# Optimization experiments

Hardware: AMD Instinct MI355X
Metric: run time of the kernel (lower is better)

The kernel has to match this reference:

```python
import jax, jax.numpy as jnp
import numpy as np

N_NODES = 100000
N_EDGES = 1600000
N_GRAPHS = 512
NUM_REL = 3


def setup_inputs() -> dict:
    key = jax.random.key(0)
    ks = jax.random.split(key, 16)
    shape_idx = jax.random.randint(ks[0], (N_NODES,), 0, 16)
    color_idx = jax.random.randint(ks[1], (N_NODES,), 0, 8)
    node_feats = jnp.stack([shape_idx, color_idx], axis=1)  # [N,2] int
    edge_index = jax.random.randint(ks[2], (2, N_EDGES), 0, N_NODES)
    edge_type = jax.random.randint(ks[3], (N_EDGES,), 0, NUM_REL)
    batch = jnp.sort(jax.random.randint(ks[4], (N_NODES,), 0, N_GRAPHS))
    s = lambda k, sh: jax.random.normal(k, sh, dtype=jnp.float32) * 0.05
    return {
        'node_feats': node_feats,
        'edge_index': edge_index,
        'edge_type': edge_type,
        'batch': batch,
        'shape_emb': s(ks[5], (16, 8)),
        'color_emb': s(ks[6], (8, 8)),
        'pre_w': s(ks[7], (16, 32)),
        'pre_b': jnp.zeros((32,), jnp.float32),
        'root1': s(ks[8], (32, 64)),
        'rel1': s(ks[9], (NUM_REL, 32, 64)),
        'bias1': jnp.zeros((64,), jnp.float32),
        'root2': s(ks[10], (64, 64)),
        'rel2': s(ks[11], (NUM_REL, 64, 64)),
        'bias2': jnp.zeros((64,), jnp.float32),
        'cls_w': s(ks[12], (64, 10)),
        'cls_b': jnp.zeros((10,), jnp.float32),
    }


def rgcn_conv(x, edge_index, edge_type, root, rel_w, bias):
    # PyG RGCNConv: out_i = x_i @ root + sum_r mean_{j in N_r(i)} x_j @ W_r + bias
    src, dst = edge_index[0], edge_index[1]
    out = x @ root + bias
    xs = x[src]  # [E, in] gathered source features
    for r in range(NUM_REL):
        m = (edge_type == r).astype(x.dtype)  # [E]
        msg = (xs @ rel_w[r]) * m[:, None]  # [E, out]
        agg = jax.ops.segment_sum(msg, dst, num_segments=N_NODES)
        cnt = jax.ops.segment_sum(m, dst, num_segments=N_NODES)
        out = out + agg / jnp.maximum(cnt, 1.0)[:, None]
    return out


def reference(node_feats, edge_index, edge_type, batch, shape_emb, color_emb,
              pre_w, pre_b, root1, rel1, bias1, root2, rel2, bias2, cls_w, cls_b):
    x = jnp.concatenate([shape_emb[node_feats[:, 0]], color_emb[node_feats[:, 1]]], axis=1)  # [N,16]
    x = jax.nn.relu(x @ pre_w + pre_b)  # [N,32]
    x = jax.nn.relu(rgcn_conv(x, edge_index, edge_type, root1, rel1, bias1))  # [N,64]
    x = jax.nn.relu(rgcn_conv(x, edge_index, edge_type, root2, rel2, bias2))  # [N,64]
    # global_mean_pool over graph ids
    s = jax.ops.segment_sum(x, batch, num_segments=N_GRAPHS)
    c = jax.ops.segment_sum(jnp.ones((x.shape[0],), x.dtype), batch, num_segments=N_GRAPHS)
    pooled = s / jnp.maximum(c, 1.0)[:, None]  # [G,64]
    return pooled @ cls_w + cls_b  # [G,num_classes]
```

## Files before the change

kernel.cpp:

```cpp
#include <hip/hip_runtime.h>

#define NN 100000
#define NE 1600000
#define NG 512

#define BSH 9
#define NB 196
#define EPB 8192
#define NAB ((NE + EPB - 1) / EPB)
#define CAP 9216

__global__ __launch_bounds__(256) void k_embed(
    const int* __restrict__ nf, const float* __restrict__ semb,
    const float* __restrict__ cemb, const float* __restrict__ pw,
    const float* __restrict__ pb, float* __restrict__ x1)
{
  int gid = blockIdx.x * 256 + threadIdx.x;
  bool valid = gid < NN;
  int i = valid ? gid : NN - 1;
  int sf = nf[2 * i], cf = nf[2 * i + 1];
  float x0[16];
#pragma unroll
  for (int k = 0; k < 8; ++k) x0[k] = semb[sf * 8 + k];
#pragma unroll
  for (int k = 0; k < 8; ++k) x0[8 + k] = cemb[cf * 8 + k];
  float acc[32];
#pragma unroll
  for (int j = 0; j < 32; ++j) acc[j] = pb[j];
#pragma unroll
  for (int k = 0; k < 16; ++k) {
    float xv = x0[k];
#pragma unroll
    for (int j = 0; j < 32; ++j) acc[j] += xv * pw[k * 32 + j];
  }
  if (valid) {
    float4* o = (float4*)(x1 + (size_t)i * 32);
#pragma unroll
    for (int j4 = 0; j4 < 8; ++j4) {
      float4 v;
      v.x = fmaxf(acc[4 * j4 + 0], 0.f);
      v.y = fmaxf(acc[4 * j4 + 1], 0.f);
      v.z = fmaxf(acc[4 * j4 + 2], 0.f);
      v.w = fmaxf(acc[4 * j4 + 3], 0.f);
      o[j4] = v;
    }
  }
}


__global__ __launch_bounds__(256) void kA_count(
    const int* __restrict__ ei, int* __restrict__ bkt_cnt)
{
  __shared__ int lh[NB];
  for (int b = threadIdx.x; b < NB; b += 256) lh[b] = 0;
  __syncthreads();
  int base = blockIdx.x * EPB;
#pragma unroll
  for (int i = 0; i < EPB / 256; ++i) {
    int e = base + i * 256 + threadIdx.x;
    if (e < NE) atomicAdd(&lh[ei[NE + e] >> BSH], 1);
  }
  __syncthreads();
  for (int b = threadIdx.x; b < NB; b += 256)
    if (lh[b]) atomicAdd(&bkt_cnt[b], lh[b]);
}

__global__ __launch_bounds__(256) void kA_scan(
    const int* __restrict__ bkt_cnt, int* __restrict__ bkt_base,
    int* __restrict__ bkt_cur)
{
  __shared__ int sm[2][256];
  int t = threadIdx.x;
  int v = (t < NB) ? bkt_cnt[t] : 0;
  sm[0][t] = v;
  __syncthreads();
  int cur = 0;
#pragma unroll
  for (int off = 1; off < 256; off <<= 1) {
    int add = (t >= off) ? sm[cur][t - off] : 0;
    sm[cur ^ 1][t] = sm[cur][t] + add;
    __syncthreads();
    cur ^= 1;
  }
  if (t < NB) {
    int ex = sm[cur][t] - v;
    bkt_base[t] = ex;
    bkt_cur[t] = ex;
  }
  if (t == 0) bkt_base[NB] = NE;
}

__global__ __launch_bounds__(256) void kA_scatter(
    const int* __restrict__ ei, const int* __restrict__ et,
    int* __restrict__ bkt_cur, int* __restrict__ binned)
{
  __shared__ int packA[EPB];
  __shared__ unsigned char bktA[EPB];
  __shared__ int lh[NB], grun[NB], lcur[NB];
  for (int b = threadIdx.x; b < NB; b += 256) { lh[b] = 0; lcur[b] = 0; }
  __syncthreads();
  int base = blockIdx.x * EPB;
#pragma unroll
  for (int i = 0; i < EPB / 256; ++i) {
    int p = i * 256 + threadIdx.x;
    int e = base + p;
    if (e < NE) {
      int src = ei[e], dst = ei[NE + e], ty = et[e];
      int b = dst >> BSH;
      packA[p] = src | (ty << 17) | ((dst & 511) << 19);
      bktA[p] = (unsigned char)b;
      atomicAdd(&lh[b], 1);
    } else {
      bktA[p] = 255;
    }
  }
  __syncthreads();
  for (int b = threadIdx.x; b < NB; b += 256)
    grun[b] = lh[b] ? atomicAdd(&bkt_cur[b], lh[b]) : 0;
  __syncthreads();
#pragma unroll
  for (int i = 0; i < EPB / 256; ++i) {
    int p = i * 256 + threadIdx.x;
    int b = bktA[p];
    if (b != 255) {
      int off = atomicAdd(&lcur[b], 1);
      binned[grun[b] + off] = packA[p];
    }
  }
}

__global__ __launch_bounds__(512) void kB_build(
    const int* __restrict__ bkt_base, const int* __restrict__ binned,
    int* __restrict__ rs3, int* __restrict__ ep)
{
  __shared__ int stage[CAP];
  __shared__ int ldeg3[1536], lrs3[1536], lcur3[1536];
  __shared__ int sm[2][512];
  int b = blockIdx.x;
  int t = threadIdx.x;
  int p0 = bkt_base[b], p1 = bkt_base[b + 1];
  int cnt = p1 - p0;
  int nodes0 = b << BSH;
  int nnodes = NN - nodes0 < 512 ? NN - nodes0 : 512;
  ldeg3[t] = 0; ldeg3[t + 512] = 0; ldeg3[t + 1024] = 0;
  lcur3[t] = 0; lcur3[t + 512] = 0; lcur3[t + 1024] = 0;
  __syncthreads();
  for (int p = t; p < cnt; p += 512) {
    int pk = binned[p0 + p];
    if (p < CAP) stage[p] = pk;
    int key = ((pk >> 19) & 511) * 3 + ((pk >> 17) & 3);
    atomicAdd(&ldeg3[key], 1);
  }
  __syncthreads();
  int s0 = ldeg3[3 * t], s1 = ldeg3[3 * t + 1], s2 = ldeg3[3 * t + 2];
  int tot = s0 + s1 + s2;
  sm[0][t] = tot;
  __syncthreads();
  int cur = 0;
#pragma unroll
  for (int off = 1; off < 512; off <<= 1) {
    int add = (t >= off) ? sm[cur][t - off] : 0;
    sm[cur ^ 1][t] = sm[cur][t] + add;
    __syncthreads();
    cur ^= 1;
  }
  int ex = sm[cur][t] - tot;
  int r0 = p0 + ex, r1 = r0 + s0, r2 = r1 + s1;
  lrs3[3 * t] = r0;
  lrs3[3 * t + 1] = r1;
  lrs3[3 * t + 2] = r2;
  if (t < nnodes) {
    size_t base3 = (size_t)(nodes0 + t) * 3;
    rs3[base3 + 0] = r0;
    rs3[base3 + 1] = r1;
    rs3[base3 + 2] = r2;
  }
  if (b == NB - 1 && t == 0) rs3[(size_t)NN * 3] = NE;
  __syncthreads();
  for (int p = t; p < cnt; p += 512) {
    int pk = (p < CAP) ? stage[p] : binned[p0 + p];
    int key = ((pk >> 19) & 511) * 3 + ((pk >> 17) & 3);
    int off = atomicAdd(&lcur3[key], 1);
    ep[lrs3[key] + off] = pk & 0x1FFFF;
  }
}

template <int IN>
__global__ __launch_bounds__(512) void k_fused(
    const float* __restrict__ x, const int* __restrict__ rs3,
    const int* __restrict__ ep, const float* __restrict__ root,
    const float* __restrict__ rel, const float* __restrict__ bias,
    float* __restrict__ y)
{
  __shared__ float smem[3 * IN][65];
  const int tid = threadIdx.x;
  const int node0 = blockIdx.x * 64;
  const int wv = tid >> 6;
  const int lane = tid & 63;

  constexpr int LPE = IN / 4;
  constexpr int DPW = (IN == 32) ? 2 : 1;
  constexpr int SW = 64 / DPW;
  constexpr int EPI = SW / LPE;
  const int sub = (IN == 64) ? 0 : (lane >> 5);
  const int sl = lane % SW;
  const int k4 = sl % LPE;
  const int es = sl / LPE;

  for (int it = 0; it < 8 / DPW; ++it) {
    int dl = wv * 8 + it * DPW + sub;
    int d = node0 + dl;
    int q0 = 0, q1 = 0, q2 = 0, q3 = 0;
    if (d < NN) {
      q0 = rs3[3 * d + 0];
      q1 = rs3[3 * d + 1];
      q2 = rs3[3 * d + 2];
      q3 = rs3[3 * d + 3];
    }
    float4 a0 = make_float4(0.f, 0.f, 0.f, 0.f);
    float4 a1 = make_float4(0.f, 0.f, 0.f, 0.f);
    float4 a2 = make_float4(0.f, 0.f, 0.f, 0.f);
#pragma unroll 2
    for (int p = q0; p < q3; p += EPI) {
      int idx = p + es;
      bool val = idx < q3;
      int e = ep[val ? idx : q3 - 1];
      float4 v = *(const float4*)(x + (size_t)e * IN + k4 * 4);
      float m0 = (val && idx < q1) ? 1.f : 0.f;
      float m1 = (val && idx >= q1 && idx < q2) ? 1.f : 0.f;
      float m2 = (val && idx >= q2) ? 1.f : 0.f;
      a0.x = fmaf(m0, v.x, a0.x); a0.y = fmaf(m0, v.y, a0.y);
      a0.z = fmaf(m0, v.z, a0.z); a0.w = fmaf(m0, v.w, a0.w);
      a1.x = fmaf(m1, v.x, a1.x); a1.y = fmaf(m1, v.y, a1.y);
      a1.z = fmaf(m1, v.z, a1.z); a1.w = fmaf(m1, v.w, a1.w);
      a2.x = fmaf(m2, v.x, a2.x); a2.y = fmaf(m2, v.y, a2.y);
      a2.z = fmaf(m2, v.z, a2.z); a2.w = fmaf(m2, v.w, a2.w);
    }
#pragma unroll
    for (int off = LPE; off < SW; off <<= 1) {
      a0.x += __shfl_xor(a0.x, off, 64); a0.y += __shfl_xor(a0.y, off, 64);
      a0.z += __shfl_xor(a0.z, off, 64); a0.w += __shfl_xor(a0.w, off, 64);
      a1.x += __shfl_xor(a1.x, off, 64); a1.y += __shfl_xor(a1.y, off, 64);
      a1.z += __shfl_xor(a1.z, off, 64); a1.w += __shfl_xor(a1.w, off, 64);
      a2.x += __shfl_xor(a2.x, off, 64); a2.y += __shfl_xor(a2.y, off, 64);
      a2.z += __shfl_xor(a2.z, off, 64); a2.w += __shfl_xor(a2.w, off, 64);
    }
    if (es == 0) {
      float c0 = (float)(q1 - q0 > 0 ? q1 - q0 : 1);
      float c1 = (float)(q2 - q1 > 0 ? q2 - q1 : 1);
      float c2 = (float)(q3 - q2 > 0 ? q3 - q2 : 1);
      int r0 = k4 * 4;
      smem[0 * IN + r0 + 0][dl] = a0.x / c0;
      smem[0 * IN + r0 + 1][dl] = a0.y / c0;
      smem[0 * IN + r0 + 2][dl] = a0.z / c0;
      smem[0 * IN + r0 + 3][dl] = a0.w / c0;
      smem[1 * IN + r0 + 0][dl] = a1.x / c1;
      smem[1 * IN + r0 + 1][dl] = a1.y / c1;
      smem[1 * IN + r0 + 2][dl] = a1.z / c1;
      smem[1 * IN + r0 + 3][dl] = a1.w / c1;
      smem[2 * IN + r0 + 0][dl] = a2.x / c2;
      smem[2 * IN + r0 + 1][dl] = a2.y / c2;
      smem[2 * IN + r0 + 2][dl] = a2.z / c2;
      smem[2 * IN + r0 + 3][dl] = a2.w / c2;
    }
  }
  __syncthreads();

  const int n = lane;
  const int j0 = __builtin_amdgcn_readfirstlane(wv * 8);
  constexpr int F4 = IN / 4;
  constexpr int NPF = (64 * F4) / 512;

  float4 pf[NPF];
#pragma unroll
  for (int u = 0; u < NPF; ++u) {
    int idx = u * 512 + tid;
    int nn = idx / F4, c4 = idx % F4;
    int node = node0 + nn;
    pf[u] = make_float4(0.f, 0.f, 0.f, 0.f);
    if (node < NN) pf[u] = *(const float4*)(x + (size_t)node * IN + c4 * 4);
  }

  float acc[8];
#pragma unroll
  for (int j = 0; j < 8; ++j) acc[j] = bias[j0 + j];

  auto mm = [&](const float* __restrict__ W, int row0) {
#pragma unroll 4
    for (int k = 0; k < IN; ++k) {
      float sk = smem[row0 + k][n];
      const float* w = W + (size_t)k * 64 + j0;
#pragma unroll
      for (int j = 0; j < 8; ++j) acc[j] = fmaf(sk, w[j], acc[j]);
    }
  };

  mm(rel, 0);
  mm(rel + (size_t)IN * 64, IN);
  mm(rel + (size_t)2 * IN * 64, 2 * IN);
  __syncthreads();

#pragma unroll
  for (int u = 0; u < NPF; ++u) {
    int idx = u * 512 + tid;
    int nn = idx / F4, c4 = idx % F4;
    smem[c4 * 4 + 0][nn] = pf[u].x;
    smem[c4 * 4 + 1][nn] = pf[u].y;
    smem[c4 * 4 + 2][nn] = pf[u].z;
    smem[c4 * 4 + 3][nn] = pf[u].w;
  }
  __syncthreads();
  mm(root, 0);

  int node = node0 + n;
  if (node < NN) {
    float4* o = (float4*)(y + (size_t)node * 64 + j0);
    float4 v;
    v.x = fmaxf(acc[0], 0.f); v.y = fmaxf(acc[1], 0.f);
    v.z = fmaxf(acc[2], 0.f); v.w = fmaxf(acc[3], 0.f);
    o[0] = v;
    v.x = fmaxf(acc[4], 0.f); v.y = fmaxf(acc[5], 0.f);
    v.z = fmaxf(acc[6], 0.f); v.w = fmaxf(acc[7], 0.f);
    o[1] = v;
  }
}

__global__ __launch_bounds__(256) void k_pool(
    const float* __restrict__ x3, const int* __restrict__ batch,
    float* __restrict__ pooled, float* __restrict__ gcnt)
{
  int gwave = (blockIdx.x * 256 + threadIdx.x) >> 6;
  int lane = threadIdx.x & 63;
  int n0 = gwave * 64;
  if (n0 >= NN) return;
  int n1 = n0 + 64 < NN ? n0 + 64 : NN;
  int gcur = batch[n0];
  float acc = 0.f;
  int run = 0;
  for (int n = n0; n < n1; ++n) {
    int g = batch[n];
    if (g != gcur) {
      atomicAdd(&pooled[gcur * 64 + lane], acc);
      if (lane == 0) atomicAdd(&gcnt[gcur], (float)run);
      acc = 0.f; run = 0; gcur = g;
    }
    acc += x3[(size_t)n * 64 + lane];
    ++run;
  }
  atomicAdd(&pooled[gcur * 64 + lane], acc);
  if (lane == 0) atomicAdd(&gcnt[gcur], (float)run);
}

__global__ __launch_bounds__(256) void k_cls(
    const float* __restrict__ pooled, const float* __restrict__ gcnt,
    const float* __restrict__ cw, const float* __restrict__ cb, float* __restrict__ out)
{
  int t = blockIdx.x * 256 + threadIdx.x;
  if (t >= NG * 10) return;
  int g = t / 10, c = t % 10;
  float cf = fmaxf(gcnt[g], 1.f);
  float acc = cb[c];
#pragma unroll 8
  for (int k = 0; k < 64; ++k)
    acc += (pooled[g * 64 + k] / cf) * cw[k * 10 + c];
  out[t] = acc;
}

extern "C" void kernel_launch(void* const* d_in, const int* in_sizes, int n_in,
                              void* d_out, int out_size, void* d_ws, size_t ws_size,
                              hipStream_t stream)
{
  const int* nf = (const int*)d_in[0];
  const int* ei = (const int*)d_in[1];
  const int* et = (const int*)d_in[2];
  const int* batch = (const int*)d_in[3];
  const float* semb = (const float*)d_in[4];
  const float* cemb = (const float*)d_in[5];
  const float* pw = (const float*)d_in[6];
  const float* pb = (const float*)d_in[7];
  const float* root1 = (const float*)d_in[8];
  const float* rel1 = (const float*)d_in[9];
  const float* bias1 = (const float*)d_in[10];
  const float* root2 = (const float*)d_in[11];
  const float* rel2 = (const float*)d_in[12];
  const float* bias2 = (const float*)d_in[13];
  const float* cw = (const float*)d_in[14];
  const float* cb = (const float*)d_in[15];
  float* out = (float*)d_out;

  char* ws = (char*)d_ws;
  size_t off = 0;
  auto alloc = [&](size_t bytes) {
    char* p = ws + off;
    off += (bytes + 255) & ~(size_t)255;
    return p;
  };
  int* bkt_cnt = (int*)alloc((size_t)NB * 4);
  int* bkt_base = (int*)alloc((size_t)(NB + 1) * 4);
  int* bkt_cur = (int*)alloc((size_t)NB * 4);
  int* rs3 = (int*)alloc(((size_t)NN * 3 + 1) * 4);
  int* ep = (int*)alloc((size_t)NE * 4 + 256);
  int* binned = (int*)alloc((size_t)NE * 4);
  float* xA = (float*)alloc((size_t)NN * 64 * 4);
  float* xB = (float*)alloc((size_t)NN * 64 * 4);
  float* pooled = (float*)alloc((size_t)NG * 64 * 4);
  float* gcnt = (float*)alloc((size_t)NG * 4);
  (void)ws_size; (void)in_sizes; (void)n_in; (void)out_size;

  hipMemsetAsync(bkt_cnt, 0, (size_t)NB * 4, stream);
  k_embed<<<(NN + 255) / 256, 256, 0, stream>>>(nf, semb, cemb, pw, pb, xB);

  kA_count<<<NAB, 256, 0, stream>>>(ei, bkt_cnt);
  kA_scan<<<1, 256, 0, stream>>>(bkt_cnt, bkt_base, bkt_cur);
  kA_scatter<<<NAB, 256, 0, stream>>>(ei, et, bkt_cur, binned);
  kB_build<<<NB, 512, 0, stream>>>(bkt_base, binned, rs3, ep);

  int fgrid = (NN + 63) / 64;

  k_fused<32><<<fgrid, 512, 0, stream>>>(xB, rs3, ep, root1, rel1, bias1, xA);
  k_fused<64><<<fgrid, 512, 0, stream>>>(xA, rs3, ep, root2, rel2, bias2, xB);

  hipMemsetAsync(pooled, 0, (size_t)NG * 64 * 4, stream);
  hipMemsetAsync(gcnt, 0, (size_t)NG * 4, stream);
  int nwaves = (NN + 63) / 64;
  k_pool<<<(nwaves + 3) / 4, 256, 0, stream>>>(xB, batch, pooled, gcnt);
  k_cls<<<(NG * 10 + 255) / 256, 256, 0, stream>>>(pooled, gcnt, cw, cb, out);
}
```

Before: 289.0 us.

## Replace count/scan binning with fixed-capacity buckets and shuffle-broadcast edge indices

```diff
diff --git a/kernel.cpp b/kernel.cpp
--- a/kernel.cpp
+++ b/kernel.cpp
@@ -8,6 +8,7 @@
 #define NB 196
 #define EPB 8192
 #define NAB ((NE + EPB - 1) / EPB)
+#define CAPB 9216
 #define CAP 9216
 
 __global__ __launch_bounds__(256) void k_embed(
@@ -47,48 +48,6 @@
   }
 }
 
-
-__global__ __launch_bounds__(256) void kA_count(
-    const int* __restrict__ ei, int* __restrict__ bkt_cnt)
-{
-  __shared__ int lh[NB];
-  for (int b = threadIdx.x; b < NB; b += 256) lh[b] = 0;
-  __syncthreads();
-  int base = blockIdx.x * EPB;
-#pragma unroll
-  for (int i = 0; i < EPB / 256; ++i) {
-    int e = base + i * 256 + threadIdx.x;
-    if (e < NE) atomicAdd(&lh[ei[NE + e] >> BSH], 1);
-  }
-  __syncthreads();
-  for (int b = threadIdx.x; b < NB; b += 256)
-    if (lh[b]) atomicAdd(&bkt_cnt[b], lh[b]);
-}
-
-__global__ __launch_bounds__(256) void kA_scan(
-    const int* __restrict__ bkt_cnt, int* __restrict__ bkt_base,
-    int* __restrict__ bkt_cur)
-{
-  __shared__ int sm[2][256];
-  int t = threadIdx.x;
-  int v = (t < NB) ? bkt_cnt[t] : 0;
-  sm[0][t] = v;
-  __syncthreads();
-  int cur = 0;
-#pragma unroll
-  for (int off = 1; off < 256; off <<= 1) {
-    int add = (t >= off) ? sm[cur][t - off] : 0;
-    sm[cur ^ 1][t] = sm[cur][t] + add;
-    __syncthreads();
-    cur ^= 1;
-  }
-  if (t < NB) {
-    int ex = sm[cur][t] - v;
-    bkt_base[t] = ex;
-    bkt_cur[t] = ex;
-  }
-  if (t == 0) bkt_base[NB] = NE;
-}
 
 __global__ __launch_bounds__(256) void kA_scatter(
     const int* __restrict__ ei, const int* __restrict__ et,
@@ -123,23 +82,24 @@
     int p = i * 256 + threadIdx.x;
     int b = bktA[p];
     if (b != 255) {
-      int off = atomicAdd(&lcur[b], 1);
-      binned[grun[b] + off] = packA[p];
+      int off = grun[b] + atomicAdd(&lcur[b], 1);
+      if (off < CAPB) binned[b * CAPB + off] = packA[p];
     }
   }
 }
 
 __global__ __launch_bounds__(512) void kB_build(
-    const int* __restrict__ bkt_base, const int* __restrict__ binned,
-    int* __restrict__ rs3, int* __restrict__ ep)
+    const int* __restrict__ bkt_cur, const int* __restrict__ binned,
+    int* __restrict__ rs4, int* __restrict__ ep)
 {
   __shared__ int stage[CAP];
   __shared__ int ldeg3[1536], lrs3[1536], lcur3[1536];
   __shared__ int sm[2][512];
   int b = blockIdx.x;
   int t = threadIdx.x;
-  int p0 = bkt_base[b], p1 = bkt_base[b + 1];
-  int cnt = p1 - p0;
+  int p0 = b * CAPB;
+  int cnt = bkt_cur[b];
+  if (cnt > CAPB) cnt = CAPB;
   int nodes0 = b << BSH;
   int nnodes = NN - nodes0 < 512 ? NN - nodes0 : 512;
   ldeg3[t] = 0; ldeg3[t + 512] = 0; ldeg3[t + 1024] = 0;
@@ -170,12 +130,8 @@
   lrs3[3 * t + 1] = r1;
   lrs3[3 * t + 2] = r2;
   if (t < nnodes) {
-    size_t base3 = (size_t)(nodes0 + t) * 3;
-    rs3[base3 + 0] = r0;
-    rs3[base3 + 1] = r1;
-    rs3[base3 + 2] = r2;
-  }
-  if (b == NB - 1 && t == 0) rs3[(size_t)NN * 3] = NE;
+    *(int4*)(rs4 + (size_t)4 * (nodes0 + t)) = make_int4(r0, r1, r2, r2 + s2);
+  }
   __syncthreads();
   for (int p = t; p < cnt; p += 512) {
     int pk = (p < CAP) ? stage[p] : binned[p0 + p];
@@ -187,7 +143,7 @@
 
 template <int IN>
 __global__ __launch_bounds__(512) void k_fused(
-    const float* __restrict__ x, const int* __restrict__ rs3,
+    const float* __restrict__ x, const int* __restrict__ rs4,
     const int* __restrict__ ep, const float* __restrict__ root,
     const float* __restrict__ rel, const float* __restrict__ bias,
     float* __restrict__ y)
@@ -203,38 +159,40 @@
   constexpr int SW = 64 / DPW;
   constexpr int EPI = SW / LPE;
   const int sub = (IN == 64) ? 0 : (lane >> 5);
-  const int sl = lane % SW;
+  const int sl = lane & (SW - 1);
   const int k4 = sl % LPE;
   const int es = sl / LPE;
+  const int subBase = lane & ~(SW - 1);
 
   for (int it = 0; it < 8 / DPW; ++it) {
     int dl = wv * 8 + it * DPW + sub;
     int d = node0 + dl;
-    int q0 = 0, q1 = 0, q2 = 0, q3 = 0;
-    if (d < NN) {
-      q0 = rs3[3 * d + 0];
-      q1 = rs3[3 * d + 1];
-      q2 = rs3[3 * d + 2];
-      q3 = rs3[3 * d + 3];
-    }
+    int4 q = make_int4(0, 0, 0, 0);
+    if (d < NN) q = *(const int4*)(rs4 + (size_t)4 * d);
+    const int q0 = q.x, q1 = q.y, q2 = q.z, q3 = q.w;
     float4 a0 = make_float4(0.f, 0.f, 0.f, 0.f);
     float4 a1 = make_float4(0.f, 0.f, 0.f, 0.f);
     float4 a2 = make_float4(0.f, 0.f, 0.f, 0.f);
-#pragma unroll 2
-    for (int p = q0; p < q3; p += EPI) {
-      int idx = p + es;
-      bool val = idx < q3;
-      int e = ep[val ? idx : q3 - 1];
-      float4 v = *(const float4*)(x + (size_t)e * IN + k4 * 4);
-      float m0 = (val && idx < q1) ? 1.f : 0.f;
-      float m1 = (val && idx >= q1 && idx < q2) ? 1.f : 0.f;
-      float m2 = (val && idx >= q2) ? 1.f : 0.f;
-      a0.x = fmaf(m0, v.x, a0.x); a0.y = fmaf(m0, v.y, a0.y);
-      a0.z = fmaf(m0, v.z, a0.z); a0.w = fmaf(m0, v.w, a0.w);
-      a1.x = fmaf(m1, v.x, a1.x); a1.y = fmaf(m1, v.y, a1.y);
-      a1.z = fmaf(m1, v.z, a1.z); a1.w = fmaf(m1, v.w, a1.w);
-      a2.x = fmaf(m2, v.x, a2.x); a2.y = fmaf(m2, v.y, a2.y);
-      a2.z = fmaf(m2, v.z, a2.z); a2.w = fmaf(m2, v.w, a2.w);
+    for (int base = q0; base < q3; base += SW) {
+      int epv = ep[base + sl];
+      int pend = (base + SW < q3) ? base + SW : q3;
+#pragma unroll 4
+      for (int p = base; p < pend; p += EPI) {
+        int idx = p + es;
+        bool val = idx < pend;
+        int srcLane = subBase | ((idx - base) & (SW - 1));
+        int e = __shfl(epv, srcLane, 64);
+        float4 v = *(const float4*)(x + (size_t)e * IN + k4 * 4);
+        float m0 = (val && idx < q1) ? 1.f : 0.f;
+        float m1 = (val && idx >= q1 && idx < q2) ? 1.f : 0.f;
+        float m2 = (val && idx >= q2) ? 1.f : 0.f;
+        a0.x = fmaf(m0, v.x, a0.x); a0.y = fmaf(m0, v.y, a0.y);
+        a0.z = fmaf(m0, v.z, a0.z); a0.w = fmaf(m0, v.w, a0.w);
+        a1.x = fmaf(m1, v.x, a1.x); a1.y = fmaf(m1, v.y, a1.y);
+        a1.z = fmaf(m1, v.z, a1.z); a1.w = fmaf(m1, v.w, a1.w);
+        a2.x = fmaf(m2, v.x, a2.x); a2.y = fmaf(m2, v.y, a2.y);
+        a2.z = fmaf(m2, v.z, a2.z); a2.w = fmaf(m2, v.w, a2.w);
+      }
     }
 #pragma unroll
     for (int off = LPE; off < SW; off <<= 1) {
@@ -395,30 +353,27 @@
     off += (bytes + 255) & ~(size_t)255;
     return p;
   };
-  int* bkt_cnt = (int*)alloc((size_t)NB * 4);
-  int* bkt_base = (int*)alloc((size_t)(NB + 1) * 4);
   int* bkt_cur = (int*)alloc((size_t)NB * 4);
-  int* rs3 = (int*)alloc(((size_t)NN * 3 + 1) * 4);
-  int* ep = (int*)alloc((size_t)NE * 4 + 256);
-  int* binned = (int*)alloc((size_t)NE * 4);
+  int* rs4 = (int*)alloc((size_t)NN * 4 * 4);
+  int* ep = (int*)alloc(((size_t)NB * CAPB + 64) * 4);
+  int* binned = (int*)alloc((size_t)NB * CAPB * 4);
   float* xA = (float*)alloc((size_t)NN * 64 * 4);
   float* xB = (float*)alloc((size_t)NN * 64 * 4);
   float* pooled = (float*)alloc((size_t)NG * 64 * 4);
   float* gcnt = (float*)alloc((size_t)NG * 4);
   (void)ws_size; (void)in_sizes; (void)n_in; (void)out_size;
 
-  hipMemsetAsync(bkt_cnt, 0, (size_t)NB * 4, stream);
+  hipMemsetAsync(bkt_cur, 0, (size_t)NB * 4, stream);
+  hipMemsetAsync(ep, 0, ((size_t)NB * CAPB + 64) * 4, stream);
   k_embed<<<(NN + 255) / 256, 256, 0, stream>>>(nf, semb, cemb, pw, pb, xB);
 
-  kA_count<<<NAB, 256, 0, stream>>>(ei, bkt_cnt);
-  kA_scan<<<1, 256, 0, stream>>>(bkt_cnt, bkt_base, bkt_cur);
   kA_scatter<<<NAB, 256, 0, stream>>>(ei, et, bkt_cur, binned);
-  kB_build<<<NB, 512, 0, stream>>>(bkt_base, binned, rs3, ep);
+  kB_build<<<NB, 512, 0, stream>>>(bkt_cur, binned, rs4, ep);
 
   int fgrid = (NN + 63) / 64;
 
-  k_fused<32><<<fgrid, 512, 0, stream>>>(xB, rs3, ep, root1, rel1, bias1, xA);
-  k_fused<64><<<fgrid, 512, 0, stream>>>(xA, rs3, ep, root2, rel2, bias2, xB);
+  k_fused<32><<<fgrid, 512, 0, stream>>>(xB, rs4, ep, root1, rel1, bias1, xA);
+  k_fused<64><<<fgrid, 512, 0, stream>>>(xA, rs4, ep, root2, rel2, bias2, xB);
 
   hipMemsetAsync(pooled, 0, (size_t)NG * 64 * 4, stream);
   hipMemsetAsync(gcnt, 0, (size_t)NG * 4, stream);
```

Result: no change. 287.4 us (-0.6%).
